# Kernel optimization log

Hardware: AMD Instinct MI355X
Metric: run time of the kernel (lower is better)

## Reference

```python
import jax, jax.numpy as jnp
import numpy as np

N = 50000   # nodes
E = 800000  # edges (avg degree 16)
IN = 256    # in_dim
H = 4       # nhead
D = 64      # out_dim per head
NEG_SLOPE_ATTN = 0.2   # DGL GATConv default negative_slope for edge scores
NEG_SLOPE_OUT = 0.01   # nn.LeakyReLU default on the layer output


def setup_inputs() -> dict:
    key = jax.random.key(0)
    ks = jax.random.split(key, 6)
    h = jax.random.normal(ks[0], (N, IN), dtype=jnp.float32)
    src = jax.random.randint(ks[1], (E,), 0, N, dtype=jnp.int32)
    dst = jax.random.randint(ks[2], (E,), 0, N, dtype=jnp.int32)
    W = jax.random.normal(ks[3], (IN, H * D), dtype=jnp.float32) / np.float32(np.sqrt(IN))
    attn_l = jax.random.normal(ks[4], (H, D), dtype=jnp.float32) * 0.1
    attn_r = jax.random.normal(ks[5], (H, D), dtype=jnp.float32) * 0.1
    bias = jnp.zeros((H * D,), dtype=jnp.float32)
    return {"h": h, "src": src, "dst": dst, "W": W,
            "attn_l": attn_l, "attn_r": attn_r, "bias": bias}


def reference(h, src, dst, W, attn_l, attn_r, bias):
    n = h.shape[0]
    # linear projection -> [N, H, D]
    feat = (h @ W).reshape(n, H, D)
    # per-node, per-head attention halves: [N, H]
    el = jnp.sum(feat * attn_l, axis=-1)
    er = jnp.sum(feat * attn_r, axis=-1)
    # per-edge unnormalized score (DGL: src contributes el, dst contributes er)
    e = jax.nn.leaky_relu(el[src] + er[dst], NEG_SLOPE_ATTN)  # [E, H]
    # edge softmax over incoming edges of each destination node
    emax = jax.ops.segment_max(e, dst, num_segments=n)        # [N, H]
    ee = jnp.exp(e - emax[dst])                               # [E, H]
    denom = jax.ops.segment_sum(ee, dst, num_segments=n)      # [N, H]
    a = ee / jnp.maximum(denom[dst], 1e-9)                    # [E, H]
    # weighted scatter-aggregate of projected source features
    msg = feat[src] * a[:, :, None]                           # [E, H, D]
    rst = jax.ops.segment_sum(msg, dst, num_segments=n)       # [N, H, D]
    rst = rst + bias.reshape(H, D)
    # outer activation (dropout is identity in eval)
    return jax.nn.leaky_relu(rst, NEG_SLOPE_OUT)
```

## Files before the change

kernel.cpp:

```cpp
#include <hip/hip_runtime.h>

#define IN_DIM 256
#define HD 256
#define NHEAD 4
#define BM 128

typedef __attribute__((ext_vector_type(8))) short short8;
typedef __attribute__((ext_vector_type(4))) float f32x4;

__device__ __forceinline__ float bf2f(ushort u) {
    unsigned x = ((unsigned)u) << 16;
    float f;
    __builtin_memcpy(&f, &x, 4);
    return f;
}
__device__ __forceinline__ ushort f2bf(float f) {
    unsigned x;
    __builtin_memcpy(&x, &f, 4);
    unsigned r = (x + 0x7FFFu + ((x >> 16) & 1u)) >> 16;
    return (ushort)r;
}
__device__ __forceinline__ short8 cvt8(float4 x, float4 y) {
    short8 a;
    a[0] = (short)f2bf(x.x); a[1] = (short)f2bf(x.y);
    a[2] = (short)f2bf(x.z); a[3] = (short)f2bf(x.w);
    a[4] = (short)f2bf(y.x); a[5] = (short)f2bf(y.y);
    a[6] = (short)f2bf(y.z); a[7] = (short)f2bf(y.w);
    return a;
}

__global__ void fill_one(float* __restrict__ out, int n) {
    int i = blockIdx.x * 256 + threadIdx.x;
    if (i < n) out[i] = 1.0f;
}

__global__ void conv_w_zero(const float* __restrict__ W, ushort* __restrict__ WT,
                            int* __restrict__ cnt, int* __restrict__ donecnt, int n) {
    int idx = blockIdx.x * 256 + threadIdx.x;
    int k = idx >> 8, c = idx & 255;
    WT[c * 256 + k] = f2bf(W[idx]);
    for (int i = idx; i < n; i += 65536) cnt[i] = 0;
    if (idx == 0) *donecnt = 0;
}

__global__ __launch_bounds__(256, 2) void gemm_hist(const float* __restrict__ h,
                                                    const short* __restrict__ WT,
                                                    ushort* __restrict__ featb,
                                                    float* __restrict__ el,
                                                    float* __restrict__ er,
                                                    const float* __restrict__ attn_l,
                                                    const float* __restrict__ attn_r,
                                                    const int* __restrict__ dst,
                                                    int* __restrict__ cnt,
                                                    int* __restrict__ epos,
                                                    int n, int e4, int e) {
    __shared__ __align__(16) ushort blds[2][8192];
    int t = threadIdx.x;
    int w = t >> 6, l = t & 63;
    int c15 = l & 15, g = l >> 4;
    int blockBase = blockIdx.x * BM;
    int row0 = blockBase + w * 32 + c15;
    int rA0 = row0 < n ? row0 : n - 1;
    int rA1 = (row0 + 16) < n ? (row0 + 16) : n - 1;
    const float* hA0 = h + (size_t)rA0 * 256 + g * 8;
    const float* hA1 = h + (size_t)rA1 * 256 + g * 8;

    f32x4 acc[2][16];
#pragma unroll
    for (int af = 0; af < 2; ++af)
#pragma unroll
        for (int ct = 0; ct < 16; ++ct) acc[af][ct] = (f32x4)(0.0f);

    short8 st[4];
    int sc[4], sb[4];
#pragma unroll
    for (int p = 0; p < 4; ++p) {
        int q = t + p * 256;
        sc[p] = q >> 2;
        int gg = q & 3;
        sb[p] = ((sc[p] * 64 + gg * 16) ^ ((sc[p] & 7) << 4));
    }

#pragma unroll
    for (int p = 0; p < 4; ++p)
        st[p] = *(const short8*)(WT + sc[p] * 256 + ((t + p * 256) & 3) * 8);
#pragma unroll
    for (int p = 0; p < 4; ++p)
        *(short8*)((char*)blds[0] + sb[p]) = st[p];
    __syncthreads();

    for (int kk = 0; kk < 8; ++kk) {
        int buf = kk & 1;
        if (kk < 7) {
#pragma unroll
            for (int p = 0; p < 4; ++p)
                st[p] = *(const short8*)(WT + sc[p] * 256 + (kk + 1) * 32 + ((t + p * 256) & 3) * 8);
        }
        float4 x0 = *(const float4*)(hA0 + kk * 32);
        float4 y0 = *(const float4*)(hA0 + kk * 32 + 4);
        float4 x1 = *(const float4*)(hA1 + kk * 32);
        float4 y1 = *(const float4*)(hA1 + kk * 32 + 4);
        short8 a0 = cvt8(x0, y0);
        short8 a1 = cvt8(x1, y1);
        const char* bb = (const char*)blds[buf];
#pragma unroll
        for (int ct = 0; ct < 16; ++ct) {
            int c = ct * 16 + c15;
            short8 bv = *(const short8*)(bb + ((c * 64 + g * 16) ^ ((c & 7) << 4)));
            acc[0][ct] = __builtin_amdgcn_mfma_f32_16x16x32_bf16(a0, bv, acc[0][ct], 0, 0, 0);
            acc[1][ct] = __builtin_amdgcn_mfma_f32_16x16x32_bf16(a1, bv, acc[1][ct], 0, 0, 0);
        }
        if (kk < 7) {
#pragma unroll
            for (int p = 0; p < 4; ++p)
                *(short8*)((char*)blds[buf ^ 1] + sb[p]) = st[p];
        }
        __syncthreads();
    }

    float alv[16], arv[16];
#pragma unroll
    for (int ct = 0; ct < 16; ++ct) {
        alv[ct] = attn_l[ct * 16 + c15];
        arv[ct] = attn_r[ct * 16 + c15];
    }

#pragma unroll
    for (int af = 0; af < 2; ++af) {
        int rowb = blockBase + w * 32 + af * 16 + g * 4;
#pragma unroll
        for (int r = 0; r < 4; ++r) {
            int row = rowb + r;
            if (row < n) {
#pragma unroll
                for (int ct = 0; ct < 16; ++ct)
                    featb[(size_t)row * 256 + ct * 16 + c15] = f2bf(acc[af][ct][r]);
            }
            float pl[4] = {0.f, 0.f, 0.f, 0.f}, pr[4] = {0.f, 0.f, 0.f, 0.f};
#pragma unroll
            for (int ct = 0; ct < 16; ++ct) {
                pl[ct >> 2] += acc[af][ct][r] * alv[ct];
                pr[ct >> 2] += acc[af][ct][r] * arv[ct];
            }
#pragma unroll
            for (int m = 1; m < 16; m <<= 1) {
#pragma unroll
                for (int hh = 0; hh < 4; ++hh) {
                    pl[hh] += __shfl_xor(pl[hh], m, 64);
                    pr[hh] += __shfl_xor(pr[hh], m, 64);
                }
            }
            if (row < n) {
                if (c15 < 4)       el[row * 4 + c15]       = pl[c15];
                else if (c15 < 8)  er[row * 4 + (c15 - 4)] = pr[c15 - 4];
            }
        }
    }

    int nthreads = gridDim.x * 256;
    for (int qq = blockIdx.x * 256 + t; qq < e4; qq += nthreads) {
        int base = qq * 4;
        int4 d4 = *(const int4*)(dst + base);
        int4 p4;
        p4.x = atomicAdd(&cnt[d4.x], 1);
        p4.y = atomicAdd(&cnt[d4.y], 1);
        p4.z = atomicAdd(&cnt[d4.z], 1);
        p4.w = atomicAdd(&cnt[d4.w], 1);
        *(int4*)(epos + base) = p4;
    }
    if (blockIdx.x == 0 && t == 0) {
        for (int q = e4 * 4; q < e; ++q) epos[q] = atomicAdd(&cnt[dst[q]], 1);
    }
}

__global__ __launch_bounds__(1024) void scan_fused(const int* __restrict__ cnt,
                                                   int* __restrict__ rl,
                                                   int* __restrict__ bsum,
                                                   int* __restrict__ donecnt,
                                                   int n, int nb) {
    __shared__ int wsums[16];
    __shared__ int isLast;
    int t = threadIdx.x, lane = t & 63, wid = t >> 6;
    int i = blockIdx.x * 1024 + t;
    int x = (i < n) ? cnt[i] : 0;
    int s = x;
#pragma unroll
    for (int off = 1; off < 64; off <<= 1) {
        int v = __shfl_up(s, off, 64);
        if (lane >= off) s += v;
    }
    if (lane == 63) wsums[wid] = s;
    __syncthreads();
    if (wid == 0) {
        int ws = (lane < 16) ? wsums[lane] : 0;
#pragma unroll
        for (int off = 1; off < 16; off <<= 1) {
            int v = __shfl_up(ws, off, 64);
            if (lane >= off) ws += v;
        }
        if (lane < 16) wsums[lane] = ws;
    }
    __syncthreads();
    int woff = (wid > 0) ? wsums[wid - 1] : 0;
    if (i <= n) rl[i] = woff + s - x;
    if (t == 1023) bsum[blockIdx.x] = wsums[15];

    __threadfence();
    if (t == 0) {
        int prev = atomicAdd(donecnt, 1);
        isLast = (prev == gridDim.x - 1) ? 1 : 0;
    }
    __syncthreads();
    if (!isLast) return;
    __threadfence();
    int carry = 0;
    for (int base = 0; base < nb; base += 1024) {
        __syncthreads();
        int ii = base + t;
        int xx = (ii < nb) ? bsum[ii] : 0;
        int ss = xx;
#pragma unroll
        for (int off = 1; off < 64; off <<= 1) {
            int v = __shfl_up(ss, off, 64);
            if (lane >= off) ss += v;
        }
        if (lane == 63) wsums[wid] = ss;
        __syncthreads();
        if (wid == 0) {
            int ws = (lane < 16) ? wsums[lane] : 0;
#pragma unroll
            for (int off = 1; off < 16; off <<= 1) {
                int v = __shfl_up(ws, off, 64);
                if (lane >= off) ws += v;
            }
            if (lane < 16) wsums[lane] = ws;
        }
        __syncthreads();
        int woff2 = (wid > 0) ? wsums[wid - 1] : 0;
        if (ii < nb) bsum[ii] = carry + woff2 + ss - xx;
        int tot = wsums[15];
        carry += tot;
    }
}

__global__ void fill_kernel(const int* __restrict__ src, const int* __restrict__ dst,
                            const int* __restrict__ rl, const int* __restrict__ boffs,
                            const int* __restrict__ epos,
                            int* __restrict__ esrc, int e4, int e) {
    int nthreads = gridDim.x * 256;
    for (int i = blockIdx.x * 256 + threadIdx.x; i < e4; i += nthreads) {
        int base = i * 4;
        int4 d4 = *(const int4*)(dst + base);
        int4 s4 = *(const int4*)(src + base);
        int4 p4 = *(const int4*)(epos + base);
        int pos0 = boffs[d4.x >> 10] + rl[d4.x] + p4.x;
        int pos1 = boffs[d4.y >> 10] + rl[d4.y] + p4.y;
        int pos2 = boffs[d4.z >> 10] + rl[d4.z] + p4.z;
        int pos3 = boffs[d4.w >> 10] + rl[d4.w] + p4.w;
        if (pos0 >= 0 && pos0 < e) esrc[pos0] = s4.x;
        if (pos1 >= 0 && pos1 < e) esrc[pos1] = s4.y;
        if (pos2 >= 0 && pos2 < e) esrc[pos2] = s4.z;
        if (pos3 >= 0 && pos3 < e) esrc[pos3] = s4.w;
    }
    if (blockIdx.x == 0 && threadIdx.x == 0) {
        for (int q = e4 * 4; q < e; ++q) {
            int d = dst[q];
            int pos = boffs[d >> 10] + rl[d] + epos[q];
            if (pos >= 0 && pos < e) esrc[pos] = src[q];
        }
    }
}

__global__ __launch_bounds__(64) void aggregate(const int* __restrict__ rl,
                                                const int* __restrict__ boffs,
                                                const int* __restrict__ esrc,
                                                const float* __restrict__ el,
                                                const float* __restrict__ er,
                                                const ushort* __restrict__ featb,
                                                const float* __restrict__ bias,
                                                float* __restrict__ out, int n) {
    __shared__ int sbuf[64];
    __shared__ float wbuf[64][4];
    int node = blockIdx.x;
    int l = threadIdx.x;
    int hh = l >> 4;
    int beg = boffs[node >> 10] + rl[node];
    int end = boffs[(node + 1) >> 10] + rl[node + 1];
    float4 bv = *(const float4*)(bias + l * 4);
    float* op = out + (size_t)node * 256 + l * 4;
    if (beg >= end) {
        float4 v;
        v.x = bv.x > 0.f ? bv.x : 0.01f * bv.x;
        v.y = bv.y > 0.f ? bv.y : 0.01f * bv.y;
        v.z = bv.z > 0.f ? bv.z : 0.01f * bv.z;
        v.w = bv.w > 0.f ? bv.w : 0.01f * bv.w;
        *(float4*)op = v;
        return;
    }
    float4 r4 = *(const float4*)(er + (size_t)node * 4);
    float ax = 0.f, ay = 0.f, az = 0.f, aw = 0.f, s = 0.f;
    for (int cb = beg; cb < end; cb += 64) {
        int cn = min(64, end - cb);
        __syncthreads();
        if (l < cn) {
            int sv = esrc[cb + l];
            sv = (sv >= 0 && sv < n) ? sv : 0;
            sbuf[l] = sv;
            float4 l4 = *(const float4*)(el + (size_t)sv * 4);
            float e0 = l4.x + r4.x; e0 = e0 > 0.f ? e0 : 0.2f * e0;
            float e1 = l4.y + r4.y; e1 = e1 > 0.f ? e1 : 0.2f * e1;
            float e2 = l4.z + r4.z; e2 = e2 > 0.f ? e2 : 0.2f * e2;
            float e3 = l4.w + r4.w; e3 = e3 > 0.f ? e3 : 0.2f * e3;
            wbuf[l][0] = __expf(fminf(e0, 60.f));
            wbuf[l][1] = __expf(fminf(e1, 60.f));
            wbuf[l][2] = __expf(fminf(e2, 60.f));
            wbuf[l][3] = __expf(fminf(e3, 60.f));
        }
        __syncthreads();
#pragma unroll 4
        for (int j = 0; j < cn; ++j) {
            int sid = sbuf[j];
            float wgt = wbuf[j][hh];
            ushort4 f4 = *(const ushort4*)(featb + (size_t)sid * 256 + l * 4);
            ax += wgt * bf2f(f4.x);
            ay += wgt * bf2f(f4.y);
            az += wgt * bf2f(f4.z);
            aw += wgt * bf2f(f4.w);
            s += wgt;
        }
    }
    float inv = 1.f / fmaxf(s, 1e-9f);
    float4 v;
    v.x = ax * inv + bv.x; v.x = v.x > 0.f ? v.x : 0.01f * v.x;
    v.y = ay * inv + bv.y; v.y = v.y > 0.f ? v.y : 0.01f * v.y;
    v.z = az * inv + bv.z; v.z = v.z > 0.f ? v.z : 0.01f * v.z;
    v.w = aw * inv + bv.w; v.w = v.w > 0.f ? v.w : 0.01f * v.w;
    *(float4*)op = v;
}

extern "C" void kernel_launch(void* const* d_in, const int* in_sizes, int n_in,
                              void* d_out, int out_size, void* d_ws, size_t ws_size,
                              hipStream_t stream) {
    const float* h      = (const float*)d_in[0];
    const int*   src    = (const int*)d_in[1];
    const int*   dst    = (const int*)d_in[2];
    const float* W      = (const float*)d_in[3];
    const float* attn_l = (const float*)d_in[4];
    const float* attn_r = (const float*)d_in[5];
    const float* bias   = (const float*)d_in[6];
    float* out = (float*)d_out;

    int N = in_sizes[0] / IN_DIM;
    int E = in_sizes[1];
    int E4 = E / 4;
    int NB = (N + 1 + 1023) / 1024;

    auto al = [](size_t x) { return (x + 255) & ~(size_t)255; };
    char* ws = (char*)d_ws;
    size_t o = 0;
    ushort* featb = (ushort*)(ws + o); o += al((size_t)N * HD * 2);
    float*  el    = (float*)(ws + o);  o += al((size_t)N * NHEAD * 4);
    float*  er    = (float*)(ws + o);  o += al((size_t)N * NHEAD * 4);
    int*    rl    = (int*)(ws + o);    o += al((size_t)(N + 1) * 4);
    int*    cnt   = (int*)(ws + o);    o += al((size_t)N * 4);
    int*    bsum  = (int*)(ws + o);    o += al((size_t)NB * 4);
    int*    done  = (int*)(ws + o);    o += al(4);
    int*    esrc  = (int*)(ws + o);    o += al((size_t)E * 4);
    int*    epos  = (int*)(ws + o);    o += al((size_t)E * 4);
    ushort* WT    = (ushort*)(ws + o); o += al((size_t)IN_DIM * HD * 2);
    (void)n_in;

    if (ws_size < o) {
        fill_one<<<(out_size + 255) / 256, 256, 0, stream>>>(out, out_size);
        return;
    }

    conv_w_zero<<<(IN_DIM * HD) / 256, 256, 0, stream>>>(W, WT, cnt, done, N);

    int GB = (N + BM - 1) / BM;
    gemm_hist<<<GB, 256, 0, stream>>>(h, (const short*)WT, featb, el, er,
                                      attn_l, attn_r, dst, cnt, epos, N, E4, E);

    scan_fused<<<NB, 1024, 0, stream>>>(cnt, rl, bsum, done, N, NB);

    int FB = (E4 + 511) / 512;
    fill_kernel<<<FB, 256, 0, stream>>>(src, dst, rl, bsum, epos, esrc, E4, E);

    aggregate<<<N, 64, 0, stream>>>(rl, bsum, esrc, el, er, featb, bias, out, N);
}
```

Baseline: 162.3 us.

## Move dst histogram into dedicated extra blocks of GEMM kernel

The destination-degree histogram, previously a grid-stride loop run by every GEMM block after its matrix tile, now runs in separate extra blocks appended to the GEMM grid, each handling one int4 of edges. These blocks can overlap with the GEMM work instead of serialising after it, and the hist blocks use few resources. The fill kernel also switches from a grid-stride loop over half as many threads to one int4 per thread, and tail edges are handled per-thread rather than by a single serial thread. The extra small blocks add scheduling overhead, and they may compete with GEMM blocks for slots.

```diff
diff --git a/kernel.cpp b/kernel.cpp
--- a/kernel.cpp
+++ b/kernel.cpp
@@ -53,7 +53,23 @@
                                                     const int* __restrict__ dst,
                                                     int* __restrict__ cnt,
                                                     int* __restrict__ epos,
-                                                    int n, int e4, int e) {
+                                                    int gb, int n, int e) {
+    if (blockIdx.x >= gb) {
+        int i = (blockIdx.x - gb) * 256 + threadIdx.x;
+        int base = i * 4;
+        if (base + 3 < e) {
+            int4 d4 = *(const int4*)(dst + base);
+            int4 p4;
+            p4.x = atomicAdd(&cnt[d4.x], 1);
+            p4.y = atomicAdd(&cnt[d4.y], 1);
+            p4.z = atomicAdd(&cnt[d4.z], 1);
+            p4.w = atomicAdd(&cnt[d4.w], 1);
+            *(int4*)(epos + base) = p4;
+        } else {
+            for (int q = base; q < e; ++q) epos[q] = atomicAdd(&cnt[dst[q]], 1);
+        }
+        return;
+    }
     __shared__ __align__(16) ushort blds[2][8192];
     int t = threadIdx.x;
     int w = t >> 6, l = t & 63;
@@ -155,21 +171,6 @@
                 else if (c15 < 8)  er[row * 4 + (c15 - 4)] = pr[c15 - 4];
             }
         }
-    }
-
-    int nthreads = gridDim.x * 256;
-    for (int qq = blockIdx.x * 256 + t; qq < e4; qq += nthreads) {
-        int base = qq * 4;
-        int4 d4 = *(const int4*)(dst + base);
-        int4 p4;
-        p4.x = atomicAdd(&cnt[d4.x], 1);
-        p4.y = atomicAdd(&cnt[d4.y], 1);
-        p4.z = atomicAdd(&cnt[d4.z], 1);
-        p4.w = atomicAdd(&cnt[d4.w], 1);
-        *(int4*)(epos + base) = p4;
-    }
-    if (blockIdx.x == 0 && t == 0) {
-        for (int q = e4 * 4; q < e; ++q) epos[q] = atomicAdd(&cnt[dst[q]], 1);
     }
 }
 
@@ -246,10 +247,10 @@
 __global__ void fill_kernel(const int* __restrict__ src, const int* __restrict__ dst,
                             const int* __restrict__ rl, const int* __restrict__ boffs,
                             const int* __restrict__ epos,
-                            int* __restrict__ esrc, int e4, int e) {
-    int nthreads = gridDim.x * 256;
-    for (int i = blockIdx.x * 256 + threadIdx.x; i < e4; i += nthreads) {
-        int base = i * 4;
+                            int* __restrict__ esrc, int e) {
+    int i = blockIdx.x * 256 + threadIdx.x;
+    int base = i * 4;
+    if (base + 3 < e) {
         int4 d4 = *(const int4*)(dst + base);
         int4 s4 = *(const int4*)(src + base);
         int4 p4 = *(const int4*)(epos + base);
@@ -261,9 +262,8 @@
         if (pos1 >= 0 && pos1 < e) esrc[pos1] = s4.y;
         if (pos2 >= 0 && pos2 < e) esrc[pos2] = s4.z;
         if (pos3 >= 0 && pos3 < e) esrc[pos3] = s4.w;
-    }
-    if (blockIdx.x == 0 && threadIdx.x == 0) {
-        for (int q = e4 * 4; q < e; ++q) {
+    } else {
+        for (int q = base; q < e; ++q) {
             int d = dst[q];
             int pos = boffs[d >> 10] + rl[d] + epos[q];
             if (pos >= 0 && pos < e) esrc[pos] = src[q];
@@ -352,7 +352,6 @@
 
     int N = in_sizes[0] / IN_DIM;
     int E = in_sizes[1];
-    int E4 = E / 4;
     int NB = (N + 1 + 1023) / 1024;
 
     auto al = [](size_t x) { return (x + 255) & ~(size_t)255; };
@@ -378,13 +377,13 @@
     conv_w_zero<<<(IN_DIM * HD) / 256, 256, 0, stream>>>(W, WT, cnt, done, N);
 
     int GB = (N + BM - 1) / BM;
-    gemm_hist<<<GB, 256, 0, stream>>>(h, (const short*)WT, featb, el, er,
-                                      attn_l, attn_r, dst, cnt, epos, N, E4, E);
+    int HB = ((E + 3) / 4 + 255) / 256;
+    gemm_hist<<<GB + HB, 256, 0, stream>>>(h, (const short*)WT, featb, el, er,
+                                           attn_l, attn_r, dst, cnt, epos, GB, N, E);
 
     scan_fused<<<NB, 1024, 0, stream>>>(cnt, rl, bsum, done, N, NB);
 
-    int FB = (E4 + 511) / 512;
-    fill_kernel<<<FB, 256, 0, stream>>>(src, dst, rl, bsum, epos, esrc, E4, E);
+    fill_kernel<<<((E + 3) / 4 + 255) / 256, 256, 0, stream>>>(src, dst, rl, bsum, epos, esrc, E);
 
     aggregate<<<N, 64, 0, stream>>>(rl, bsum, esrc, el, er, featb, bias, out, N);
 }
```

Result: faster. 156.6 us (-3.5%).
